# Optimization experiments

Measured on AMD Instinct MI355X. Metric: run time of the kernel, lower is better.

## Reference

```python
import jax, jax.numpy as jnp
import numpy as np

B, S, F, H = 2048, 512, 64, 256

def setup_inputs() -> dict:
    key = jax.random.key(0)
    ks = jax.random.split(key, 9)
    s = 0.05
    return {
        "x": jax.random.normal(ks[0], (B, S, F), jnp.float32),
        "h0": jax.random.normal(ks[1], (1, B, H), jnp.float32),
        "c0": jax.random.normal(ks[2], (1, B, H), jnp.float32),
        "W_ih": jax.random.normal(ks[3], (4 * H, F), jnp.float32) * s,
        "W_hh": jax.random.normal(ks[4], (4 * H, H), jnp.float32) * s,
        "b_ih": jax.random.normal(ks[5], (4 * H,), jnp.float32) * s,
        "b_hh": jax.random.normal(ks[6], (4 * H,), jnp.float32) * s,
        "W_dense": jax.random.normal(ks[7], (F, H), jnp.float32) * s,
        "b_dense": jax.random.normal(ks[8], (F,), jnp.float32) * s,
        "seq_len": S,
    }

def reference(x, h0, c0, W_ih, W_hh, b_ih, b_hh, W_dense, b_dense, seq_len):
    # h_0 tensors are [1, B, H]; original squeezes dim 0.
    h = h0[0]
    c = c0[0]
    bias = b_ih + b_hh  # [4H]
    Hd = W_hh.shape[1]

    def dense(v):  # [B, H] -> [B, F]
        return v @ W_dense.T + b_dense

    # epsilon = 0.0 => teacher forcing never used; next input is dense(c_t).
    x_t = dense(h)

    def step(carry, _):
        h, c, x_t = carry
        gates = x_t @ W_ih.T + h @ W_hh.T + bias  # [B, 4H]
        i = jax.nn.sigmoid(gates[:, 0 * Hd:1 * Hd])
        f = jax.nn.sigmoid(gates[:, 1 * Hd:2 * Hd])
        g = jnp.tanh(gates[:, 2 * Hd:3 * Hd])
        o = jax.nn.sigmoid(gates[:, 3 * Hd:4 * Hd])
        c_new = f * c + i * g
        h_new = o * jnp.tanh(c_new)
        # Original: h_t = (h', c'); x_t = dense(h_t[1]) = dense(c'); output[:, t] = dense(c')
        y = c_new @ W_dense.T + b_dense
        return (h_new, c_new, y), y

    (_, _, _), ys = jax.lax.scan(step, (h, c, x_t), None, length=seq_len)
    # ys: [S, B, F] -> [B, S, F]
    return jnp.transpose(ys, (1, 0, 2))
```

## Files before the change

kernel.cpp:

```cpp
#include <hip/hip_runtime.h>
#include <stdint.h>

#define SEQ   512
#define FD    64
#define HD    256
#define ZSTR  324
#define CSTR  260

#define GRPB      5120
#define WGB       (16 * GRPB)
#define DENSE_OFF (8 * WGB)

typedef __attribute__((ext_vector_type(8))) __bf16 bf16x8;
typedef __attribute__((ext_vector_type(4))) float  f32x4;

__device__ __forceinline__ float sigm(float x) {
    return __builtin_amdgcn_rcpf(1.0f + __expf(-x));
}
__device__ __forceinline__ float tanh_(float x) {
    return 2.0f * __builtin_amdgcn_rcpf(1.0f + __expf(-2.0f * x)) - 1.0f;
}

__global__ __launch_bounds__(64) void prep_weights(
    const float* __restrict__ W_ih, const float* __restrict__ W_hh,
    const float* __restrict__ W_dense, __bf16* __restrict__ wsb)
{
    const int b = blockIdx.x, l = threadIdx.x, lr = l & 15, lg = l >> 4;
    if (b < 128) {
        const int w = b >> 4, i = b & 15;
        const int s = 2 * w + (i >> 3), h = (i >> 2) & 1, nt = i & 3;
        const int n = nt * 256 + s * 16 + lr;
        for (int c = 0; c < 5; ++c) {
            const int k0 = h * 160 + c * 32 + lg * 8;
            const float* src = (k0 < 64) ? (W_ih + n * 64 + k0)
                                         : (W_hh + n * 256 + (k0 - 64));
            bf16x8 v;
            for (int e = 0; e < 8; ++e) v[e] = (__bf16)src[e];
            *(bf16x8*)(wsb + (size_t)((w * 16 + i) * 5 + c) * 512 + l * 8) = v;
        }
    } else {
        const int d = b - 128;
        const int f = d * 16 + lr;
        for (int c = 0; c < 8; ++c) {
            const float* src = W_dense + f * 256 + c * 32 + lg * 8;
            bf16x8 v;
            for (int e = 0; e < 8; ++e) v[e] = (__bf16)src[e];
            *(bf16x8*)(wsb + DENSE_OFF / 2 + d * 4096 + c * 512 + l * 8) = v;
        }
    }
}

__global__ __launch_bounds__(512) __attribute__((amdgpu_waves_per_eu(2, 2)))
void lstm_persist(
    const float* __restrict__ h0, const float* __restrict__ c0,
    const float* __restrict__ b_ih, const float* __restrict__ b_hh,
    const float* __restrict__ b_dense, const __bf16* __restrict__ wsb,
    float* __restrict__ out)
{
    __shared__ __align__(16) __bf16 Zb[2 * 16 * ZSTR];
    __shared__ __align__(16) __bf16 CBb[16 * CSTR];

    const int tid = threadIdx.x;
    const int w   = tid >> 6;
    const int l   = tid & 63;
    const int lr  = l & 15;
    const int lg  = l >> 4;
    const int row0 = blockIdx.x * 16;

    const __bf16* wgbase = wsb + (size_t)w * (WGB / 2);
    const __bf16* wdbase = wsb + DENSE_OFF / 2 + w * 4096 + l * 8;

    float biasv[2][4];
    float creg[2][4];
#pragma unroll
    for (int p = 0; p < 2; ++p) {
        const int jj = (2 * w + p) * 16 + lr;
#pragma unroll
        for (int nt = 0; nt < 4; ++nt) {
            const int n = nt * 256 + jj;
            biasv[p][nt] = b_ih[n] + b_hh[n];
        }
#pragma unroll
        for (int r = 0; r < 4; ++r)
            creg[p][r] = c0[(size_t)(row0 + lg * 4 + r) * HD + jj];
    }
    float ybias = (w < 4) ? b_dense[w * 16 + lr] : 0.0f;

    {
        const int e0 = tid * 8;
        const int m  = e0 >> 8;
        const int j8 = e0 & 255;
        const float4 h1 = *(const float4*)(h0 + (size_t)(row0 + m) * HD + j8);
        const float4 h2 = *(const float4*)(h0 + (size_t)(row0 + m) * HD + j8 + 4);
        __bf16* zp = &Zb[m * ZSTR + 64 + j8];
        zp[0] = (__bf16)h1.x; zp[1] = (__bf16)h1.y; zp[2] = (__bf16)h1.z; zp[3] = (__bf16)h1.w;
        zp[4] = (__bf16)h2.x; zp[5] = (__bf16)h2.y; zp[6] = (__bf16)h2.z; zp[7] = (__bf16)h2.w;
    }
    __syncthreads();

    if (w < 4) {
        f32x4 ya = {ybias, ybias, ybias, ybias};
#pragma unroll
        for (int c = 0; c < 8; ++c) {
            bf16x8 wdc = *(const bf16x8*)(wdbase + c * 512);
            bf16x8 av  = *(const bf16x8*)(&Zb[lr * ZSTR + 64 + c * 32 + lg * 8]);
            ya = __builtin_amdgcn_mfma_f32_16x16x32_bf16(av, wdc, ya, 0, 0, 0);
        }
#pragma unroll
        for (int r = 0; r < 4; ++r)
            Zb[(lg * 4 + r) * ZSTR + w * 16 + lr] = (__bf16)ya[r];
    }

    float* outp = out + (size_t)row0 * SEQ * FD;

    for (int t = 0; t < SEQ; ++t) {
        __syncthreads();

        const __bf16* Zc = Zb + (t & 1) * (16 * ZSTR);
        __bf16*       Zn = Zb + ((t + 1) & 1) * (16 * ZSTR);

        const __bf16* gp = wgbase + l * 8;
        asm volatile("" : "+v"(gp));

        bf16x8 sA[5], sB[5];
#pragma unroll
        for (int c = 0; c < 5; ++c) sA[c] = *(const bf16x8*)(gp + c * 512);
#pragma unroll
        for (int c = 0; c < 5; ++c) sB[c] = *(const bf16x8*)(gp + 2560 + c * 512);

        bf16x8 aph[5];
        f32x4  acc[4];

#pragma unroll
        for (int i = 0; i < 16; ++i) {
            const int p = i >> 3, h = (i >> 2) & 1, nt = i & 3;

            if ((i & 3) == 0) {
#pragma unroll
                for (int c = 0; c < 5; ++c)
                    aph[c] = *(const bf16x8*)(&Zc[lr * ZSTR + (h * 5 + c) * 32 + lg * 8]);
            }

            const float bb = biasv[p][nt];
            f32x4 cc = (h == 0) ? f32x4{bb, bb, bb, bb} : acc[nt];
            if ((i & 1) == 0) {
                cc = __builtin_amdgcn_mfma_f32_16x16x32_bf16(aph[0], sA[0], cc, 0, 0, 0);
                cc = __builtin_amdgcn_mfma_f32_16x16x32_bf16(aph[1], sA[1], cc, 0, 0, 0);
                cc = __builtin_amdgcn_mfma_f32_16x16x32_bf16(aph[2], sA[2], cc, 0, 0, 0);
                cc = __builtin_amdgcn_mfma_f32_16x16x32_bf16(aph[3], sA[3], cc, 0, 0, 0);
                cc = __builtin_amdgcn_mfma_f32_16x16x32_bf16(aph[4], sA[4], cc, 0, 0, 0);
                if (i + 2 < 16) {
#pragma unroll
                    for (int c = 0; c < 5; ++c)
                        sA[c] = *(const bf16x8*)(gp + (i + 2) * 2560 + c * 512);
                }
            } else {
                cc = __builtin_amdgcn_mfma_f32_16x16x32_bf16(aph[0], sB[0], cc, 0, 0, 0);
                cc = __builtin_amdgcn_mfma_f32_16x16x32_bf16(aph[1], sB[1], cc, 0, 0, 0);
                cc = __builtin_amdgcn_mfma_f32_16x16x32_bf16(aph[2], sB[2], cc, 0, 0, 0);
                cc = __builtin_amdgcn_mfma_f32_16x16x32_bf16(aph[3], sB[3], cc, 0, 0, 0);
                cc = __builtin_amdgcn_mfma_f32_16x16x32_bf16(aph[4], sB[4], cc, 0, 0, 0);
                if (i + 2 < 16) {
#pragma unroll
                    for (int c = 0; c < 5; ++c)
                        sB[c] = *(const bf16x8*)(gp + (i + 2) * 2560 + c * 512);
                }
            }
            acc[nt] = cc;

            if ((i & 7) == 7) {
                const int jj = (2 * w + p) * 16 + lr;
#pragma unroll
                for (int r = 0; r < 4; ++r) {
                    const int m = lg * 4 + r;
                    const float ig = sigm(acc[0][r]);
                    const float fg = sigm(acc[1][r]);
                    const float gg = tanh_(acc[2][r]);
                    const float og = sigm(acc[3][r]);
                    const float cn = fg * creg[p][r] + ig * gg;
                    creg[p][r] = cn;
                    const float hn = og * tanh_(cn);
                    Zn[m * ZSTR + 64 + jj] = (__bf16)hn;
                    CBb[m * CSTR + jj]     = (__bf16)cn;
                }
            }
        }

        __syncthreads();

        if (w < 4) {
            const __bf16* wdp = wdbase;
            asm volatile("" : "+v"(wdp));
            f32x4 ya = {ybias, ybias, ybias, ybias};
#pragma unroll
            for (int c = 0; c < 8; ++c) {
                bf16x8 wdc = *(const bf16x8*)(wdp + c * 512);
                bf16x8 acb = *(const bf16x8*)(&CBb[lr * CSTR + c * 32 + lg * 8]);
                ya = __builtin_amdgcn_mfma_f32_16x16x32_bf16(acb, wdc, ya, 0, 0, 0);
            }
            const int f = w * 16 + lr;
#pragma unroll
            for (int r = 0; r < 4; ++r) {
                const int m = lg * 4 + r;
                outp[(size_t)m * (SEQ * FD) + t * FD + f] = ya[r];
                Zn[m * ZSTR + f] = (__bf16)ya[r];
            }
        }
    }
}

extern "C" void kernel_launch(void* const* d_in, const int* in_sizes, int n_in,
                              void* d_out, int out_size, void* d_ws, size_t ws_size,
                              hipStream_t stream) {
    (void)in_sizes; (void)n_in; (void)ws_size; (void)out_size;
    const float* h0      = (const float*)d_in[1];
    const float* c0      = (const float*)d_in[2];
    const float* W_ih    = (const float*)d_in[3];
    const float* W_hh    = (const float*)d_in[4];
    const float* b_ih    = (const float*)d_in[5];
    const float* b_hh    = (const float*)d_in[6];
    const float* W_dense = (const float*)d_in[7];
    const float* b_dense = (const float*)d_in[8];
    __bf16* wsb = (__bf16*)d_ws;

    prep_weights<<<132, 64, 0, stream>>>(W_ih, W_hh, W_dense, wsb);
    lstm_persist<<<128, 512, 0, stream>>>(h0, c0, b_ih, b_hh, b_dense, wsb, (float*)d_out);
}
```

Measured before the change: 3.820 ms.

## Triple-buffer streamed gate weights with inline-asm loads and explicit vmcnt waits

Replaces the double-buffered compiler-generated weight loads in the per-timestep gate GEMM with a three-register-set rotation. Loads are issued as inline global_load_dwordx4 two groups ahead, and each group is gated by an explicit s_waitcnt vmcnt plus a sched_barrier. The aim is to keep more global loads in flight and stop the compiler from inserting conservative waits that stall the MFMA chain. The extra buffer adds register pressure under the 2-waves-per-EU budget, and the hand-coded wait counts must stay exactly matched to the issue order.

```diff
diff --git a/kernel.cpp b/kernel.cpp
--- a/kernel.cpp
+++ b/kernel.cpp
@@ -20,6 +20,17 @@
 __device__ __forceinline__ float tanh_(float x) {
     return 2.0f * __builtin_amdgcn_rcpf(1.0f + __expf(-2.0f * x)) - 1.0f;
 }
+
+__device__ __forceinline__ void gload(bf16x8& dst, const __bf16* p) {
+    asm volatile("global_load_dwordx4 %0, %1, off" : "=v"(dst) : "v"(p));
+}
+
+#define WAITBUF(B, CNT) do {                                                        \
+    asm volatile("s_waitcnt vmcnt(" CNT ")"                                         \
+        : "+v"((B)[0]), "+v"((B)[1]), "+v"((B)[2]), "+v"((B)[3]), "+v"((B)[4])      \
+        :: "memory");                                                               \
+    __builtin_amdgcn_sched_barrier(0);                                              \
+} while (0)
 
 __global__ __launch_bounds__(64) void prep_weights(
     const float* __restrict__ W_ih, const float* __restrict__ W_hh,
@@ -122,69 +133,81 @@
         const __bf16* gp = wgbase + l * 8;
         asm volatile("" : "+v"(gp));
 
-        bf16x8 sA[5], sB[5];
-#pragma unroll
-        for (int c = 0; c < 5; ++c) sA[c] = *(const bf16x8*)(gp + c * 512);
-#pragma unroll
-        for (int c = 0; c < 5; ++c) sB[c] = *(const bf16x8*)(gp + 2560 + c * 512);
-
+        bf16x8 R0[5], R1[5], R2[5];
         bf16x8 aph[5];
         f32x4  acc[4];
 
 #pragma unroll
-        for (int i = 0; i < 16; ++i) {
-            const int p = i >> 3, h = (i >> 2) & 1, nt = i & 3;
-
-            if ((i & 3) == 0) {
-#pragma unroll
-                for (int c = 0; c < 5; ++c)
-                    aph[c] = *(const bf16x8*)(&Zc[lr * ZSTR + (h * 5 + c) * 32 + lg * 8]);
-            }
-
-            const float bb = biasv[p][nt];
-            f32x4 cc = (h == 0) ? f32x4{bb, bb, bb, bb} : acc[nt];
-            if ((i & 1) == 0) {
-                cc = __builtin_amdgcn_mfma_f32_16x16x32_bf16(aph[0], sA[0], cc, 0, 0, 0);
-                cc = __builtin_amdgcn_mfma_f32_16x16x32_bf16(aph[1], sA[1], cc, 0, 0, 0);
-                cc = __builtin_amdgcn_mfma_f32_16x16x32_bf16(aph[2], sA[2], cc, 0, 0, 0);
-                cc = __builtin_amdgcn_mfma_f32_16x16x32_bf16(aph[3], sA[3], cc, 0, 0, 0);
-                cc = __builtin_amdgcn_mfma_f32_16x16x32_bf16(aph[4], sA[4], cc, 0, 0, 0);
-                if (i + 2 < 16) {
-#pragma unroll
-                    for (int c = 0; c < 5; ++c)
-                        sA[c] = *(const bf16x8*)(gp + (i + 2) * 2560 + c * 512);
-                }
-            } else {
-                cc = __builtin_amdgcn_mfma_f32_16x16x32_bf16(aph[0], sB[0], cc, 0, 0, 0);
-                cc = __builtin_amdgcn_mfma_f32_16x16x32_bf16(aph[1], sB[1], cc, 0, 0, 0);
-                cc = __builtin_amdgcn_mfma_f32_16x16x32_bf16(aph[2], sB[2], cc, 0, 0, 0);
-                cc = __builtin_amdgcn_mfma_f32_16x16x32_bf16(aph[3], sB[3], cc, 0, 0, 0);
-                cc = __builtin_amdgcn_mfma_f32_16x16x32_bf16(aph[4], sB[4], cc, 0, 0, 0);
-                if (i + 2 < 16) {
-#pragma unroll
-                    for (int c = 0; c < 5; ++c)
-                        sB[c] = *(const bf16x8*)(gp + (i + 2) * 2560 + c * 512);
-                }
-            }
-            acc[nt] = cc;
-
-            if ((i & 7) == 7) {
-                const int jj = (2 * w + p) * 16 + lr;
-#pragma unroll
-                for (int r = 0; r < 4; ++r) {
-                    const int m = lg * 4 + r;
-                    const float ig = sigm(acc[0][r]);
-                    const float fg = sigm(acc[1][r]);
-                    const float gg = tanh_(acc[2][r]);
-                    const float og = sigm(acc[3][r]);
-                    const float cn = fg * creg[p][r] + ig * gg;
-                    creg[p][r] = cn;
-                    const float hn = og * tanh_(cn);
-                    Zn[m * ZSTR + 64 + jj] = (__bf16)hn;
-                    CBb[m * CSTR + jj]     = (__bf16)cn;
-                }
-            }
-        }
+        for (int c = 0; c < 5; ++c) gload(R0[c], gp + c * 512);
+#pragma unroll
+        for (int c = 0; c < 5; ++c) gload(R1[c], gp + 2560 + c * 512);
+
+#define APH_LOAD(H) {                                                              \
+    _Pragma("unroll")                                                              \
+    for (int c = 0; c < 5; ++c)                                                    \
+        aph[c] = *(const bf16x8*)(&Zc[lr * ZSTR + ((H) * 5 + c) * 32 + lg * 8]); }
+
+#define ISSUE(G, B) {                                                              \
+    _Pragma("unroll")                                                              \
+    for (int c = 0; c < 5; ++c) gload(B[c], gp + (G) * 2560 + c * 512); }
+
+#define ELEM(P) {                                                                  \
+    const int jj = (2 * w + (P)) * 16 + lr;                                        \
+    _Pragma("unroll")                                                              \
+    for (int r = 0; r < 4; ++r) {                                                  \
+        const int m = lg * 4 + r;                                                  \
+        const float ig = sigm(acc[0][r]);                                          \
+        const float fg = sigm(acc[1][r]);                                          \
+        const float gg = tanh_(acc[2][r]);                                         \
+        const float og = sigm(acc[3][r]);                                          \
+        const float cn = fg * creg[(P)][r] + ig * gg;                              \
+        creg[(P)][r] = cn;                                                         \
+        const float hn = og * tanh_(cn);                                           \
+        Zn[m * ZSTR + 64 + jj] = (__bf16)hn;                                       \
+        CBb[m * CSTR + jj]     = (__bf16)cn;                                       \
+    } }
+
+#define GSTEP(I, BCUR, BNXT, CNT) {                                                \
+    if (((I) & 3) == 0) APH_LOAD(((I) >> 2) & 1)                                   \
+    if ((I) + 2 < 16)   ISSUE((I) + 2, BNXT)                                       \
+    WAITBUF(BCUR, CNT);                                                            \
+    f32x4 cc;                                                                      \
+    if ((((I) >> 2) & 1) == 0) {                                                   \
+        const float bb = biasv[(I) >> 3][(I) & 3];                                 \
+        cc = f32x4{bb, bb, bb, bb};                                                \
+    } else {                                                                       \
+        cc = acc[(I) & 3];                                                         \
+    }                                                                              \
+    cc = __builtin_amdgcn_mfma_f32_16x16x32_bf16(aph[0], BCUR[0], cc, 0, 0, 0);    \
+    cc = __builtin_amdgcn_mfma_f32_16x16x32_bf16(aph[1], BCUR[1], cc, 0, 0, 0);    \
+    cc = __builtin_amdgcn_mfma_f32_16x16x32_bf16(aph[2], BCUR[2], cc, 0, 0, 0);    \
+    cc = __builtin_amdgcn_mfma_f32_16x16x32_bf16(aph[3], BCUR[3], cc, 0, 0, 0);    \
+    cc = __builtin_amdgcn_mfma_f32_16x16x32_bf16(aph[4], BCUR[4], cc, 0, 0, 0);    \
+    acc[(I) & 3] = cc; }
+
+        GSTEP(0,  R0, R2, "10")
+        GSTEP(1,  R1, R0, "10")
+        GSTEP(2,  R2, R1, "10")
+        GSTEP(3,  R0, R2, "10")
+        GSTEP(4,  R1, R0, "10")
+        GSTEP(5,  R2, R1, "10")
+        GSTEP(6,  R0, R2, "10")
+        GSTEP(7,  R1, R0, "10")
+        ELEM(0)
+        GSTEP(8,  R2, R1, "10")
+        GSTEP(9,  R0, R2, "10")
+        GSTEP(10, R1, R0, "10")
+        GSTEP(11, R2, R1, "10")
+        GSTEP(12, R0, R2, "10")
+        GSTEP(13, R1, R0, "10")
+        GSTEP(14, R2, R1, "5")
+        GSTEP(15, R0, R2, "0")
+        ELEM(1)
+
+#undef GSTEP
+#undef ELEM
+#undef ISSUE
+#undef APH_LOAD
 
         __syncthreads();
 
```

New measurement: 3.291 ms. -13.8%, faster.
